# Kernel optimization log

Hardware: AMD Instinct MI355X
Metric: run time of the kernel (lower is better)

The kernel has to match this reference:

```python
import jax, jax.numpy as jnp
import numpy as np

K = 7  # window_size from init


def setup_inputs() -> dict:
    key = jax.random.key(0)
    k1, k2, k3 = jax.random.split(key, 3)
    B, S, C, H, W = 2, 5, 256, 200, 200
    hidden = max(C // 16, 4)  # 16
    feats = jax.random.normal(k1, (B, S, C, H, W), dtype=jnp.float32)
    w1 = jax.random.normal(k2, (hidden, C), dtype=jnp.float32) * (1.0 / np.sqrt(C))
    b1 = jnp.zeros((hidden,), dtype=jnp.float32)
    w2 = jax.random.normal(k3, (1, hidden), dtype=jnp.float32) * (1.0 / np.sqrt(hidden))
    b2 = jnp.zeros((1,), dtype=jnp.float32)
    return {"feats": feats, "w1": w1, "b1": b1, "w2": w2, "b2": b2}


def reference(feats, w1, b1, w2, b2):
    B, S, C, H, W = feats.shape
    pad_h = (K - H % K) % K
    pad_w = (K - W % K) % K
    x = jnp.pad(feats, ((0, 0), (0, 0), (0, 0), (0, pad_h), (0, pad_w)))
    Hp, Wp = H + pad_h, W + pad_w
    Hb, Wb = Hp // K, Wp // K
    # windowed view, matching torch unfold(3,k,k).unfold(4,k,k): [B,S,C,Hb,Wb,k,k]
    xw = x.reshape(B, S, C, Hb, K, Wb, K).transpose(0, 1, 2, 3, 5, 4, 6)
    # per-window channel descriptor: mean over the k x k window
    g = xw.mean(axis=(-1, -2))                      # [B,S,C,Hb,Wb]
    g = g.transpose(0, 1, 3, 4, 2)                  # [B,S,Hb,Wb,C]
    h = jax.nn.relu(jnp.einsum('bshwc,dc->bshwd', g, w1) + b1)
    logits = jnp.einsum('bshwd,od->bshwo', h, w2) + b2
    logits = logits[..., 0]                         # [B,S,Hb,Wb]
    # NOTE: faithful to source: softmax over dim=-1 (Wb axis), not the slice axis
    weights = jax.nn.softmax(logits, axis=-1)       # [B,S,Hb,Wb]
    # weighted sum over slices
    fused = jnp.einsum('bschwij,bshw->bchwij', xw, weights)  # [B,C,Hb,Wb,k,k]
    # faithful reassembly: permute(0,1,4,2,5,3) -> [B,C,k,Hb,k,Wb], then reshape
    fused = fused.transpose(0, 1, 4, 2, 5, 3).reshape(B, C, Hp, Wp)
    return fused[:, :, :H, :W]
```

## Files before the change

### kernel.cpp

```cpp
#include <hip/hip_runtime.h>
#include <math.h>

constexpr int B = 2, S = 5, C = 256, H = 200, W = 200;
constexpr int KW = 7;
constexpr int HB = 29, WB = 29;
constexpr int HID = 16;
constexpr int NW = HB * WB;

__global__ __launch_bounds__(512) void k_winsum(const float* __restrict__ feats,
                                                float* __restrict__ gsum) {
    const int blk = (int)blockIdx.x;
    const float* src = feats + (size_t)blk * (H * W);

    __shared__ float colg[HB * W];

    const int tid = (int)threadIdx.x;

    float4 a[3];
    int hbv[3], x4v[3];
    bool act[3];
#pragma unroll
    for (int k = 0; k < 3; ++k) {
        int q = tid + k * 512;
        act[k] = q < HB * (W / 4);
        hbv[k] = q / (W / 4);
        x4v[k] = q - hbv[k] * (W / 4);
        a[k] = make_float4(0.f, 0.f, 0.f, 0.f);
    }
#pragma unroll
    for (int i = 0; i < KW; ++i) {
#pragma unroll
        for (int k = 0; k < 3; ++k) {
            if (act[k]) {
                int y = hbv[k] * KW + i;
                if (y < H) {
                    float4 v = ((const float4*)(src + (size_t)y * W))[x4v[k]];
                    a[k].x += v.x; a[k].y += v.y; a[k].z += v.z; a[k].w += v.w;
                }
            }
        }
    }
#pragma unroll
    for (int k = 0; k < 3; ++k)
        if (act[k]) ((float4*)(colg + hbv[k] * W))[x4v[k]] = a[k];
    __syncthreads();

    float* dst = gsum + (size_t)blk * NW;
    for (int p = tid; p < NW; p += 512) {
        int hb = p / WB;
        int wb = p - hb * WB;
        int x0 = wb * KW;
        float s = 0.f;
#pragma unroll
        for (int j = 0; j < KW; ++j) {
            int x = x0 + j;
            if (x < W) s += colg[hb * W + x];
        }
        dst[p] = s;
    }
}

__global__ __launch_bounds__(256) void k_weights(const float* __restrict__ gsum,
                                                 const float* __restrict__ w1,
                                                 const float* __restrict__ b1,
                                                 const float* __restrict__ w2,
                                                 const float* __restrict__ b2,
                                                 float* __restrict__ weights) {
    int blk = blockIdx.x;
    int hb = blk % HB; blk /= HB;
    int s  = blk % S;
    int b  = blk / S;
    const int bs = b * S + s;

    __shared__ float w1s[HID * C];
    __shared__ float part[8 * HID * WB];
    __shared__ float lg[WB];

    const int tid = (int)threadIdx.x;
    for (int i = tid; i < HID * C; i += 256) w1s[i] = w1[i];
    __syncthreads();

    if (tid < 8 * WB) {
        const int cg = tid / WB;
        const int wb = tid - cg * WB;
        float acc[HID];
#pragma unroll
        for (int d = 0; d < HID; ++d) acc[d] = 0.f;
        const float* g = gsum + (size_t)bs * C * NW + hb * WB + wb;
        const int c0 = cg * (C / 8);
#pragma unroll 4
        for (int c = c0; c < c0 + C / 8; ++c) {
            float gc = g[(size_t)c * NW];
#pragma unroll
            for (int d = 0; d < HID; ++d) acc[d] += gc * w1s[d * C + c];
        }
#pragma unroll
        for (int d = 0; d < HID; ++d) part[(cg * HID + d) * WB + wb] = acc[d];
    }
    __syncthreads();

    if (tid < WB) {
        float logit = b2[0];
#pragma unroll
        for (int d = 0; d < HID; ++d) {
            float a = 0.f;
#pragma unroll
            for (int cg = 0; cg < 8; ++cg) a += part[(cg * HID + d) * WB + tid];
            float h = a * (1.0f / 49.0f) + b1[d];
            logit += fmaxf(h, 0.0f) * w2[d];
        }
        lg[tid] = logit;
    }
    __syncthreads();
    if (tid < WB) {
        float m = -INFINITY;
        for (int t = 0; t < WB; ++t) m = fmaxf(m, lg[t]);
        float sum = 0.f;
        for (int t = 0; t < WB; ++t) sum += expf(lg[t] - m);
        weights[(size_t)bs * NW + hb * WB + tid] = expf(lg[tid] - m) / sum;
    }
}

__global__ __launch_bounds__(512) void k_fuse(const float* __restrict__ feats,
                                              const float* __restrict__ weights,
                                              float* __restrict__ out) {
    int blk = blockIdx.x;
    const int hb = blk % HB; blk /= HB;
    const int c  = (C - 1) - (blk % C);
    const int b  = (B - 1) - (blk / C);

    __shared__ float buf[S][KW * W];
    __shared__ float wsl[S][WB];

    const int tid = (int)threadIdx.x;
    const size_t plane = (size_t)H * W;
    const size_t sstride = (size_t)C * plane;
    const float* f0 = feats + ((size_t)b * S * C + c) * plane;
    const int y_in0 = hb * KW;

    {
        float4 v[4];
        int sv[4], rv[4];
        bool act[4];
#pragma unroll
        for (int k = 0; k < 4; ++k) {
            int q = tid + k * 512;
            act[k] = q < S * 350;
            sv[k] = q / 350;
            rv[k] = q - sv[k] * 350;
            v[k] = make_float4(0.f, 0.f, 0.f, 0.f);
            if (act[k]) {
                int i = rv[k] / 50;
                if (y_in0 + i < H)
                    v[k] = ((const float4*)(f0 + (size_t)sv[k] * sstride +
                                            (size_t)y_in0 * W))[rv[k]];
            }
        }
#pragma unroll
        for (int k = 0; k < 4; ++k)
            if (act[k]) ((float4*)&buf[sv[k]][0])[rv[k]] = v[k];
    }
    if (tid < S * WB) {
        int s  = tid / WB;
        int wb = tid - s * WB;
        wsl[s][wb] = weights[((size_t)((b * S + s) * HB + hb)) * WB + wb];
    }
    __syncthreads();

    float* o = out + ((size_t)b * C + c) * plane;
    for (int p = tid; p < KW * 50; p += 512) {
        int i = p / 50;
        int y = i * HB + hb;
        if (y < H) {
            int x0 = (p - i * 50) * 4;
            float4 r4;
            float* rp = (float*)&r4;
#pragma unroll
            for (int u = 0; u < 4; ++u) {
                int x  = x0 + u;
                int j  = x / WB;
                int wb = x - j * WB;
                int x_in = wb * KW + j;
                float acc = 0.f;
                if (x_in < W) {
#pragma unroll
                    for (int s = 0; s < S; ++s)
                        acc += buf[s][i * W + x_in] * wsl[s][wb];
                }
                rp[u] = acc;
            }
            ((float4*)(o + (size_t)y * W))[x0 / 4] = r4;
        }
    }
}

extern "C" void kernel_launch(void* const* d_in, const int* in_sizes, int n_in,
                              void* d_out, int out_size, void* d_ws, size_t ws_size,
                              hipStream_t stream) {
    const float* feats = (const float*)d_in[0];
    const float* w1    = (const float*)d_in[1];
    const float* b1    = (const float*)d_in[2];
    const float* w2    = (const float*)d_in[3];
    const float* b2    = (const float*)d_in[4];
    float* out = (float*)d_out;

    float* gsum    = (float*)d_ws;
    float* weights = gsum + (size_t)B * S * C * NW;

    hipLaunchKernelGGL(k_winsum, dim3(B * S * C), dim3(512), 0, stream, feats, gsum);
    hipLaunchKernelGGL(k_weights, dim3(B * S * HB), dim3(256), 0, stream,
                       gsum, w1, b1, w2, b2, weights);
    hipLaunchKernelGGL(k_fuse, dim3(B * C * HB), dim3(512), 0, stream,
                       feats, weights, out);
}
```

Measured before the change: 172.2 us.

## Fuse window-sum and MLP weight kernels into one pass over feats

Merges the window-mean reduction and the per-window MLP/softmax into a single kernel with one block per (batch, slice, window row). Each wave sums 7-row strips for pairs of channels, reduces them horizontally in shared memory, and accumulates the 16 hidden outputs in registers, so the intermediate gsum buffer no longer goes through global memory and one launch disappears. The trade-off is far fewer blocks (290 instead of 2560) with a serial 16-step channel loop per wave, which may leave the GPU underutilized while it streams the whole feats tensor.

```diff
diff --git a/kernel.cpp b/kernel.cpp
--- a/kernel.cpp
+++ b/kernel.cpp
@@ -7,95 +7,92 @@
 constexpr int HID = 16;
 constexpr int NW = HB * WB;
 
-__global__ __launch_bounds__(512) void k_winsum(const float* __restrict__ feats,
-                                                float* __restrict__ gsum) {
+__global__ __launch_bounds__(512) void k_winweights(const float* __restrict__ feats,
+                                                    const float* __restrict__ w1,
+                                                    const float* __restrict__ b1,
+                                                    const float* __restrict__ w2,
+                                                    const float* __restrict__ b2,
+                                                    float* __restrict__ weights) {
     const int blk = (int)blockIdx.x;
-    const float* src = feats + (size_t)blk * (H * W);
-
-    __shared__ float colg[HB * W];
-
-    const int tid = (int)threadIdx.x;
-
-    float4 a[3];
-    int hbv[3], x4v[3];
-    bool act[3];
-#pragma unroll
-    for (int k = 0; k < 3; ++k) {
-        int q = tid + k * 512;
-        act[k] = q < HB * (W / 4);
-        hbv[k] = q / (W / 4);
-        x4v[k] = q - hbv[k] * (W / 4);
-        a[k] = make_float4(0.f, 0.f, 0.f, 0.f);
-    }
-#pragma unroll
-    for (int i = 0; i < KW; ++i) {
-#pragma unroll
-        for (int k = 0; k < 3; ++k) {
-            if (act[k]) {
-                int y = hbv[k] * KW + i;
-                if (y < H) {
-                    float4 v = ((const float4*)(src + (size_t)y * W))[x4v[k]];
-                    a[k].x += v.x; a[k].y += v.y; a[k].z += v.z; a[k].w += v.w;
+    const int hb = blk % HB;
+    const int bs = blk / HB;
+
+    __shared__ float w1s[HID * C];
+    __shared__ float csum[8][2][W];
+    __shared__ float red[8][WB][HID + 1];
+    __shared__ float accT[WB][HID];
+    __shared__ float lg[WB];
+
+    const int tid  = (int)threadIdx.x;
+    const int wave = tid >> 6;
+    const int lane = tid & 63;
+
+    for (int i = tid; i < HID * C; i += 512) w1s[i] = w1[i];
+    __syncthreads();
+
+    float accR[HID];
+#pragma unroll
+    for (int d = 0; d < HID; ++d) accR[d] = 0.f;
+
+    const size_t plane = (size_t)H * W;
+    const float* base = feats + (size_t)bs * C * plane;
+    const int y0 = hb * KW;
+
+    const int  ci1  = (lane >= 50) ? 1 : 0;
+    const int  sl1  = (lane >= 50) ? lane - 50 : lane;
+    const bool act2 = lane < 36;
+    const int  sl2  = lane + 14;
+    const int  wbl  = lane & 31;
+    const int  half = lane >> 5;
+
+    for (int t = 0; t < 16; ++t) {
+        const int cA = wave * 32 + 2 * t;
+        float4 a1 = make_float4(0.f, 0.f, 0.f, 0.f);
+        float4 a2 = make_float4(0.f, 0.f, 0.f, 0.f);
+        const float* sp1 = base + (size_t)(cA + ci1) * plane + 4 * sl1;
+        const float* sp2 = base + (size_t)(cA + 1)   * plane + 4 * sl2;
+#pragma unroll
+        for (int i = 0; i < KW; ++i) {
+            int y = y0 + i;
+            if (y < H) {
+                float4 v = *(const float4*)(sp1 + (size_t)y * W);
+                a1.x += v.x; a1.y += v.y; a1.z += v.z; a1.w += v.w;
+                if (act2) {
+                    float4 u = *(const float4*)(sp2 + (size_t)y * W);
+                    a2.x += u.x; a2.y += u.y; a2.z += u.z; a2.w += u.w;
                 }
             }
         }
-    }
-#pragma unroll
-    for (int k = 0; k < 3; ++k)
-        if (act[k]) ((float4*)(colg + hbv[k] * W))[x4v[k]] = a[k];
-    __syncthreads();
-
-    float* dst = gsum + (size_t)blk * NW;
-    for (int p = tid; p < NW; p += 512) {
-        int hb = p / WB;
-        int wb = p - hb * WB;
-        int x0 = wb * KW;
+        *(float4*)&csum[wave][ci1][4 * sl1] = a1;
+        if (act2) *(float4*)&csum[wave][1][4 * sl2] = a2;
+
+        if (wbl < WB) {
+            float g = 0.f;
+#pragma unroll
+            for (int j = 0; j < KW; ++j) {
+                int x = wbl * KW + j;
+                if (x < W) g += csum[wave][half][x];
+            }
+            const int cc = cA + half;
+#pragma unroll
+            for (int d = 0; d < HID; ++d) accR[d] += g * w1s[d * C + cc];
+        }
+    }
+
+#pragma unroll
+    for (int d = 0; d < HID; ++d) accR[d] += __shfl_down(accR[d], 32);
+    if (lane < WB) {
+#pragma unroll
+        for (int d = 0; d < HID; ++d) red[wave][lane][d] = accR[d];
+    }
+    __syncthreads();
+
+    if (tid < WB * HID) {
+        int wb = tid >> 4, d = tid & 15;
         float s = 0.f;
 #pragma unroll
-        for (int j = 0; j < KW; ++j) {
-            int x = x0 + j;
-            if (x < W) s += colg[hb * W + x];
-        }
-        dst[p] = s;
-    }
-}
-
-__global__ __launch_bounds__(256) void k_weights(const float* __restrict__ gsum,
-                                                 const float* __restrict__ w1,
-                                                 const float* __restrict__ b1,
-                                                 const float* __restrict__ w2,
-                                                 const float* __restrict__ b2,
-                                                 float* __restrict__ weights) {
-    int blk = blockIdx.x;
-    int hb = blk % HB; blk /= HB;
-    int s  = blk % S;
-    int b  = blk / S;
-    const int bs = b * S + s;
-
-    __shared__ float w1s[HID * C];
-    __shared__ float part[8 * HID * WB];
-    __shared__ float lg[WB];
-
-    const int tid = (int)threadIdx.x;
-    for (int i = tid; i < HID * C; i += 256) w1s[i] = w1[i];
-    __syncthreads();
-
-    if (tid < 8 * WB) {
-        const int cg = tid / WB;
-        const int wb = tid - cg * WB;
-        float acc[HID];
-#pragma unroll
-        for (int d = 0; d < HID; ++d) acc[d] = 0.f;
-        const float* g = gsum + (size_t)bs * C * NW + hb * WB + wb;
-        const int c0 = cg * (C / 8);
-#pragma unroll 4
-        for (int c = c0; c < c0 + C / 8; ++c) {
-            float gc = g[(size_t)c * NW];
-#pragma unroll
-            for (int d = 0; d < HID; ++d) acc[d] += gc * w1s[d * C + c];
-        }
-#pragma unroll
-        for (int d = 0; d < HID; ++d) part[(cg * HID + d) * WB + wb] = acc[d];
+        for (int w = 0; w < 8; ++w) s += red[w][wb][d];
+        accT[wb][d] = s;
     }
     __syncthreads();
 
@@ -103,21 +100,18 @@
         float logit = b2[0];
 #pragma unroll
         for (int d = 0; d < HID; ++d) {
-            float a = 0.f;
-#pragma unroll
-            for (int cg = 0; cg < 8; ++cg) a += part[(cg * HID + d) * WB + tid];
-            float h = a * (1.0f / 49.0f) + b1[d];
-            logit += fmaxf(h, 0.0f) * w2[d];
+            float h = accT[tid][d] * (1.0f / 49.0f) + b1[d];
+            logit += fmaxf(h, 0.f) * w2[d];
         }
         lg[tid] = logit;
     }
     __syncthreads();
     if (tid < WB) {
         float m = -INFINITY;
-        for (int t = 0; t < WB; ++t) m = fmaxf(m, lg[t]);
-        float sum = 0.f;
-        for (int t = 0; t < WB; ++t) sum += expf(lg[t] - m);
-        weights[(size_t)bs * NW + hb * WB + tid] = expf(lg[tid] - m) / sum;
+        for (int t2 = 0; t2 < WB; ++t2) m = fmaxf(m, lg[t2]);
+        float ssum = 0.f;
+        for (int t2 = 0; t2 < WB; ++t2) ssum += expf(lg[t2] - m);
+        weights[(size_t)blk * WB + tid] = expf(lg[tid] - m) / ssum;
     }
 }
 
@@ -204,12 +198,10 @@
     const float* b2    = (const float*)d_in[4];
     float* out = (float*)d_out;
 
-    float* gsum    = (float*)d_ws;
-    float* weights = gsum + (size_t)B * S * C * NW;
-
-    hipLaunchKernelGGL(k_winsum, dim3(B * S * C), dim3(512), 0, stream, feats, gsum);
-    hipLaunchKernelGGL(k_weights, dim3(B * S * HB), dim3(256), 0, stream,
-                       gsum, w1, b1, w2, b2, weights);
+    float* weights = (float*)d_ws;
+
+    hipLaunchKernelGGL(k_winweights, dim3(B * S * HB), dim3(512), 0, stream,
+                       feats, w1, b1, w2, b2, weights);
     hipLaunchKernelGGL(k_fuse, dim3(B * C * HB), dim3(512), 0, stream,
                        feats, weights, out);
 }
```

New measurement: 180.0 us. +4.5%, slower.
